# Kernel optimization log

Measured on AMD Instinct MI355X. Metric: run time of the kernel, lower is better.

The kernel has to match this reference:

```python
import jax, jax.numpy as jnp
import numpy as np

B, N, I, H, O, E, HD = 4, 2048, 32, 64, 32, 2, 2  # batch, nodes, in_dim, hidden, out, edgetypes, heads
D1 = H * HD * E  # layer-1 filter input dim (concat of all heads/edgetypes from layer 0)


def setup_inputs() -> dict:
    key = jax.random.key(0)
    ks = jax.random.split(key, 20)
    s = 0.1
    return {
        "nodes": jax.random.normal(ks[0], (B, N, I), jnp.float32),
        "edges": jax.random.normal(ks[1], (B, N, N, E), jnp.float32),
        "W_emb": jax.random.normal(ks[2], (I, H), jnp.float32) * s,
        "b_emb": jnp.zeros((H,), jnp.float32),
        "Wf0": jax.random.normal(ks[3], (E, HD, H, H), jnp.float32) * s,
        "w1_0": jax.random.normal(ks[4], (E, HD, H), jnp.float32) * s,
        "b1_0": jnp.zeros((E, HD), jnp.float32),
        "w2_0": jax.random.normal(ks[5], (E, HD, H), jnp.float32) * s,
        "b2_0": jnp.zeros((E, HD), jnp.float32),
        "bias0": jax.random.normal(ks[6], (HD, H), jnp.float32) * s,  # state_bias aliased across edgetypes (list-mult bug)
        "Wf1": jax.random.normal(ks[7], (E, HD, D1, H), jnp.float32) * s,
        "w1_1": jax.random.normal(ks[8], (E, HD, H), jnp.float32) * s,
        "b1_1": jnp.zeros((E, HD), jnp.float32),
        "w2_1": jax.random.normal(ks[9], (E, HD, H), jnp.float32) * s,
        "b2_1": jnp.zeros((E, HD), jnp.float32),
        "bias1": jax.random.normal(ks[10], (HD, H), jnp.float32) * s,
        "W_out": jax.random.normal(ks[11], (H, O), jnp.float32) * s,
        "b_out": jnp.zeros((O,), jnp.float32),
    }


def _gat_layer(state, Wf, w1, b1, w2, b2, bias, edges_t, last):
    # state: (B,N,Din); Wf: (E,HD,Din,H); edges_t: (E,B,N,N)
    Wh = jnp.einsum('bnd,ehdk->ehbnk', state, Wf)                     # (E,HD,B,N,H)
    a1 = jnp.einsum('ehbnk,ehk->ehbn', Wh, w1) + b1[:, :, None, None]
    a2 = jnp.einsum('ehbnk,ehk->ehbn', Wh, w2) + b2[:, :, None, None]
    logits = jax.nn.leaky_relu(a1[..., :, None] + a2[..., None, :], 0.2) + edges_t[:, None]
    att = jax.nn.softmax(logits, axis=-2)                             # torch softmax dim=1 (over rows)
    msg = jnp.einsum('ehbik,ehbkd->ehbid', att, Wh) + bias[None, :, None, None, :]
    if last:
        return jnp.mean(jax.nn.elu(msg), axis=(0, 1))                 # (B,N,H)
    # concat in (edgetype-major, head-minor) order, matching the python loops
    return jnp.transpose(msg, (2, 3, 0, 1, 4)).reshape(msg.shape[2], msg.shape[3], -1)


def reference(nodes, edges, W_emb, b_emb, Wf0, w1_0, b1_0, w2_0, b2_0, bias0,
              Wf1, w1_1, b1_1, w2_1, b2_1, bias1, W_out, b_out):
    edges_t = jnp.transpose(edges, (3, 0, 1, 2))                      # (E,B,N,N)
    state = nodes @ W_emb + b_emb                                     # embedding
    state = _gat_layer(state, Wf0, w1_0, b1_0, w2_0, b2_0, bias0, edges_t, last=False)
    state = _gat_layer(state, Wf1, w1_1, b1_1, w2_1, b2_1, bias1, edges_t, last=True)
    out = state @ W_out + b_out                                       # (B,N,O)
    return jnp.mean(out, axis=1)                                      # graph-level output (B,O)
```

## Files before the change

kernel.cpp:

```cpp
#include <hip/hip_runtime.h>
#include <hip/hip_bf16.h>


constexpr int B_  = 4;
constexpr int N_  = 2048;
constexpr int I_  = 32;
constexpr int H_  = 64;
constexpr int O_  = 32;
constexpr int EH_ = 4;
constexpr int D1_ = 256;
constexpr int BN_ = B_ * N_;
constexpr int NC_ = 16;
constexpr int CH_ = N_ / NC_;
constexpr int TI_ = 16;
constexpr int TK_ = 32;
constexpr int NKT_ = N_ / TK_;

typedef __bf16 bf16x8 __attribute__((ext_vector_type(8)));
typedef float floatx4 __attribute__((ext_vector_type(4)));

__device__ __forceinline__ unsigned short f2b(float f) {
    unsigned int u = __float_as_uint(f);
    return (unsigned short)((u + 0x7fffu + ((u >> 16) & 1u)) >> 16);
}
__device__ __forceinline__ float lrelu(float x) { return fmaxf(x, 0.2f * x); }

__global__ __launch_bounds__(256) void embed_kernel(
        const float* __restrict__ nodes, const float* __restrict__ W_emb,
        const float* __restrict__ b_emb, unsigned short* __restrict__ state0B) {
    int t = threadIdx.x;
    int r = t >> 6, h = t & 63;
    int bn = blockIdx.x * 4 + r;
    __shared__ float sn[4][I_];
    if (t < 4 * I_) {
        int rr = t / I_, ii = t % I_;
        sn[rr][ii] = nodes[(size_t)(blockIdx.x * 4 + rr) * I_ + ii];
    }
    __syncthreads();
    float acc = b_emb[h];
    #pragma unroll
    for (int i = 0; i < I_; ++i) acc += sn[r][i] * W_emb[i * H_ + h];
    state0B[(size_t)bn * H_ + h] = f2b(acc);
}

template <int DIN>
__global__ __launch_bounds__(256) void wf_pack_kernel(
        const float* __restrict__ Wf, unsigned short* __restrict__ WfB) {
    int o = blockIdx.x * 256 + threadIdx.x;
    int k = o & (DIN - 1);
    int n = (o / DIN) & 63;
    int c = o / (DIN * 64);
    WfB[o] = f2b(Wf[((size_t)c * DIN + k) * 64 + n]);
}

template <int DIN>
__global__ __launch_bounds__(256) void wh_a_mfma_kernel(
        const unsigned short* __restrict__ stateB, const unsigned short* __restrict__ WfB,
        const float* __restrict__ w1, const float* __restrict__ b1,
        const float* __restrict__ w2, const float* __restrict__ b2,
        unsigned short* __restrict__ WhB, float* __restrict__ a1,
        float* __restrict__ a2) {
    int t = threadIdx.x;
    int lane = t & 63, wv = t >> 6;
    int col = lane & 15, qd = lane >> 4;
    int bn0 = blockIdx.x * TI_;
    int b = bn0 >> 11;

    floatx4 acc[4] = {{0,0,0,0},{0,0,0,0},{0,0,0,0},{0,0,0,0}};
    const unsigned short* __restrict__ ap = stateB + (size_t)(bn0 + col) * DIN + qd * 8;
    const unsigned short* __restrict__ bp = WfB + ((size_t)(wv * 64 + col) * DIN + qd * 8);
    #pragma unroll
    for (int k0 = 0; k0 < DIN; k0 += 32) {
        bf16x8 af = *(const bf16x8*)(ap + k0);
        #pragma unroll
        for (int nt = 0; nt < 4; ++nt) {
            bf16x8 bf = *(const bf16x8*)(bp + (size_t)nt * 16 * DIN + k0);
            acc[nt] = __builtin_amdgcn_mfma_f32_16x16x32_bf16(af, bf, acc[nt], 0, 0, 0);
        }
    }
    int nb = ((bn0 & 2047) >> 3) + (qd >> 1);
    #pragma unroll
    for (int nt = 0; nt < 4; ++nt) {
        unsigned int lo = (unsigned int)f2b(acc[nt][0]) | ((unsigned int)f2b(acc[nt][1]) << 16);
        unsigned int hi = (unsigned int)f2b(acc[nt][2]) | ((unsigned int)f2b(acc[nt][3]) << 16);
        uint2 v = make_uint2(lo, hi);
        *(uint2*)(WhB + ((((size_t)(wv * B_ + b) * 256 + nb) * 64 + nt * 16 + col) * 8
                         + (qd & 1) * 4)) = v;
    }
    float p1[4] = {}, p2[4] = {};
    #pragma unroll
    for (int nt = 0; nt < 4; ++nt) {
        float w1n = w1[wv * H_ + nt * 16 + col];
        float w2n = w2[wv * H_ + nt * 16 + col];
        #pragma unroll
        for (int r = 0; r < 4; ++r) {
            p1[r] += acc[nt][r] * w1n;
            p2[r] += acc[nt][r] * w2n;
        }
    }
    #pragma unroll
    for (int m = 1; m < 16; m <<= 1)
        #pragma unroll
        for (int r = 0; r < 4; ++r) {
            p1[r] += __shfl_xor(p1[r], m, 64);
            p2[r] += __shfl_xor(p2[r], m, 64);
        }
    if (col == 0) {
        float b1c = b1[wv], b2c = b2[wv];
        #pragma unroll
        for (int r = 0; r < 4; ++r) {
            a1[(size_t)wv * BN_ + bn0 + qd * 4 + r] = p1[r] + b1c;
            a2[(size_t)wv * BN_ + bn0 + qd * 4 + r] = p2[r] + b2c;
        }
    }
}

__global__ __launch_bounds__(256) void stats_kernel(
        const float* __restrict__ edges, const float* __restrict__ a1,
        const float* __restrict__ a2, float* __restrict__ ps) {
    int blk = blockIdx.x;
    int jt = blk & 7;
    int ic = (blk >> 3) & (NC_ - 1);
    int b  = blk >> 7;
    int t = threadIdx.x;
    int j = jt * 256 + t;
    __shared__ float sa1[EH_][CH_];
    for (int q = t; q < EH_ * CH_; q += 256) {
        int cc = q / CH_, ii = q % CH_;
        sa1[cc][ii] = a1[(size_t)cc * BN_ + b * N_ + ic * CH_ + ii];
    }
    __syncthreads();
    float a2v[EH_], s[EH_] = {};
    #pragma unroll
    for (int cc = 0; cc < EH_; ++cc)
        a2v[cc] = a2[(size_t)cc * BN_ + b * N_ + j];
    const float2* __restrict__ ep = (const float2*)edges + ((size_t)(b * N_ + ic * CH_)) * N_ + j;
    for (int i0 = 0; i0 < CH_; i0 += 8) {
        float2 u[8];
        #pragma unroll
        for (int q = 0; q < 8; ++q) u[q] = ep[(size_t)(i0 + q) * N_];
        #pragma unroll
        for (int q = 0; q < 8; ++q) {
            #pragma unroll
            for (int cc = 0; cc < EH_; ++cc) {
                float x = sa1[cc][i0 + q] + a2v[cc];
                s[cc] += __expf(lrelu(x) + ((cc < 2) ? u[q].x : u[q].y));
            }
        }
    }
    #pragma unroll
    for (int cc = 0; cc < EH_; ++cc)
        ps[((size_t)ic * EH_ + cc) * BN_ + b * N_ + j] = s[cc];
}

__global__ __launch_bounds__(256) void combine_kernel(
        const float* __restrict__ ps, const float* __restrict__ a2,
        float2* __restrict__ za) {
    int q = blockIdx.x * 256 + threadIdx.x;
    float S = 0.f;
    #pragma unroll
    for (int ic = 0; ic < NC_; ++ic) S += ps[(size_t)ic * EH_ * BN_ + q];
    za[q] = make_float2(__logf(S), a2[q]);
}

template <int LAST>
__global__ __launch_bounds__(256, 4) void mac_kernel(
        const float* __restrict__ edges, const float* __restrict__ a1,
        const float2* __restrict__ za, const unsigned short* __restrict__ WhB,
        const float* __restrict__ bias, void* __restrict__ outv) {
    int t = threadIdx.x;
    int blk = blockIdx.x;
    int b = blk >> 7;
    int i0 = (blk & 127) * TI_;
    int lane = t & 63, wv = t >> 6;
    int ai = t >> 4;
    int ak = (t & 15) * 2;
    int qd = lane >> 4;
    int col = lane & 15;

    __shared__ unsigned short satt[2][EH_][TI_][40];
    __shared__ float2 szq[2][EH_][TK_];
    __shared__ float sred[EH_][TI_][H_];

    float a1v[EH_];
    #pragma unroll
    for (int cc = 0; cc < EH_; ++cc)
        a1v[cc] = a1[(size_t)cc * BN_ + b * N_ + i0 + ai];

    const float4* __restrict__ ep =
        (const float4*)edges + (size_t)(b * N_ + i0 + ai) * (N_ >> 1);
    float4 ev[4];
    #pragma unroll
    for (int q = 0; q < 4; ++q) ev[q] = ep[q * (TK_ >> 1) + (ak >> 1)];
    if (t < 128) {
        int cc = t >> 5, kk = t & 31;
        szq[0][cc][kk] = za[(size_t)cc * BN_ + b * N_ + kk];
    }
    const unsigned short* __restrict__ whb0 =
        WhB + (size_t)(wv * B_ + b) * (256 * 512);
    bf16x8 bcur[4], bnxt[4];
    #pragma unroll
    for (int nt = 0; nt < 4; ++nt)
        bcur[nt] = *(const bf16x8*)(whb0 + ((size_t)qd * 64 + nt * 16 + col) * 8);

    floatx4 acc[4] = {{0,0,0,0},{0,0,0,0},{0,0,0,0},{0,0,0,0}};
    __syncthreads();

    for (int kt = 0; kt < NKT_; ++kt) {
        int cur = kt & 1, nxt = cur ^ 1;
        int k0n = ((kt + 1) & (NKT_ - 1)) * TK_;
        if (t < 128) {
            int cc = t >> 5, kk = t & 31;
            szq[nxt][cc][kk] = za[(size_t)cc * BN_ + b * N_ + k0n + kk];
        }
        float4 e0 = ev[kt & 3];
        #pragma unroll
        for (int cc = 0; cc < EH_; ++cc) {
            float2 z0 = szq[cur][cc][ak];
            float2 z1 = szq[cur][cc][ak + 1];
            float ea = (cc < 2) ? e0.x : e0.y;
            float eb = (cc < 2) ? e0.z : e0.w;
            float at0 = __expf(lrelu(a1v[cc] + z0.y) + ea - z0.x);
            float at1 = __expf(lrelu(a1v[cc] + z1.y) + eb - z1.x);
            unsigned int p = (unsigned int)f2b(at0) | ((unsigned int)f2b(at1) << 16);
            *(unsigned int*)&satt[cur][cc][ai][ak] = p;
        }
        ev[kt & 3] = ep[((kt + 4) & (NKT_ - 1)) * (TK_ >> 1) + (ak >> 1)];
        __syncthreads();
        int kb = ((kt + 1) & (NKT_ - 1)) * (TK_ >> 3);
        #pragma unroll
        for (int nt = 0; nt < 4; ++nt)
            bnxt[nt] = *(const bf16x8*)(whb0 + ((size_t)(kb + qd) * 64 + nt * 16 + col) * 8);
        bf16x8 af = *(const bf16x8*)&satt[cur][wv][col][qd * 8];
        #pragma unroll
        for (int nt = 0; nt < 4; ++nt)
            acc[nt] = __builtin_amdgcn_mfma_f32_16x16x32_bf16(af, bcur[nt], acc[nt], 0, 0, 0);
        #pragma unroll
        for (int nt = 0; nt < 4; ++nt) bcur[nt] = bnxt[nt];
    }

    if (LAST) {
        float* out = (float*)outv;
        #pragma unroll
        for (int nt = 0; nt < 4; ++nt) {
            float bv = bias[(wv & 1) * H_ + nt * 16 + col];
            #pragma unroll
            for (int r = 0; r < 4; ++r) {
                float x = acc[nt][r] + bv;
                sred[wv][qd * 4 + r][nt * 16 + col] = x > 0.f ? x : (__expf(x) - 1.f);
            }
        }
        __syncthreads();
        #pragma unroll
        for (int q = 0; q < 4; ++q) {
            int p = t + q * 256;
            int r = p >> 6, d = p & 63;
            float s = sred[0][r][d] + sred[1][r][d] + sred[2][r][d] + sred[3][r][d];
            out[((size_t)(b * N_ + i0 + r)) * H_ + d] = s * 0.25f;
        }
    } else {
        unsigned short* out = (unsigned short*)outv;
        #pragma unroll
        for (int nt = 0; nt < 4; ++nt) {
            float bv = bias[(wv & 1) * H_ + nt * 16 + col];
            #pragma unroll
            for (int r = 0; r < 4; ++r)
                out[((size_t)(b * N_ + i0 + qd * 4 + r)) * D1_ + wv * H_ + nt * 16 + col] =
                    f2b(acc[nt][r] + bv);
        }
    }
}

__global__ __launch_bounds__(256) void out_kernel(
        const float* __restrict__ state2, const float* __restrict__ W_out,
        const float* __restrict__ b_out, float* __restrict__ out) {
    int b = blockIdx.x, t = threadIdx.x;
    int d = t & 63, nc = t >> 6;
    float psum = 0.f;
    const float* sp = state2 + ((size_t)b * N_ + nc * (N_ / 4)) * H_ + d;
    for (int n = 0; n < N_ / 4; ++n) psum += sp[(size_t)n * H_];
    __shared__ float red[4][H_];
    red[nc][d] = psum;
    __syncthreads();
    if (t < H_) red[0][d] = red[0][d] + red[1][d] + red[2][d] + red[3][d];
    __syncthreads();
    if (t < O_) {
        float acc = b_out[t];
        #pragma unroll 8
        for (int dd = 0; dd < H_; ++dd)
            acc += (red[0][dd] * (1.f / N_)) * W_out[dd * O_ + t];
        out[b * O_ + t] = acc;
    }
}

extern "C" void kernel_launch(void* const* d_in, const int* in_sizes, int n_in,
                              void* d_out, int out_size, void* d_ws, size_t ws_size,
                              hipStream_t stream) {
    const float* nodes = (const float*)d_in[0];
    const float* edges = (const float*)d_in[1];
    const float* W_emb = (const float*)d_in[2];
    const float* b_emb = (const float*)d_in[3];
    const float* Wf0   = (const float*)d_in[4];
    const float* w1_0  = (const float*)d_in[5];
    const float* b1_0  = (const float*)d_in[6];
    const float* w2_0  = (const float*)d_in[7];
    const float* b2_0  = (const float*)d_in[8];
    const float* bias0 = (const float*)d_in[9];
    const float* Wf1   = (const float*)d_in[10];
    const float* w1_1  = (const float*)d_in[11];
    const float* b1_1  = (const float*)d_in[12];
    const float* w2_1  = (const float*)d_in[13];
    const float* b2_1  = (const float*)d_in[14];
    const float* bias1 = (const float*)d_in[15];
    const float* W_out = (const float*)d_in[16];
    const float* b_out = (const float*)d_in[17];

    float* ws = (float*)d_ws;
    unsigned short* state0B = (unsigned short*)ws;
    unsigned short* state1B = (unsigned short*)(ws + 262144);
    float* state2 = ws + 262144 + 1048576;
    unsigned short* WhB  = (unsigned short*)(state2 + 524288);
    unsigned short* WfB0 = (unsigned short*)(state2 + 524288 + 1048576);
    unsigned short* WfB1 = WfB0 + 16384;
    float* a1   = state2 + 524288 + 1048576 + 8192 + 32768;
    float* a2   = a1 + 32768;
    float* psum = a2 + 32768;
    float2* za  = (float2*)(psum + 524288);

    wf_pack_kernel<H_><<<EH_ * 64 * H_ / 256, 256, 0, stream>>>(Wf0, WfB0);
    wf_pack_kernel<D1_><<<EH_ * 64 * D1_ / 256, 256, 0, stream>>>(Wf1, WfB1);
    embed_kernel<<<BN_ / 4, 256, 0, stream>>>(nodes, W_emb, b_emb, state0B);

    wh_a_mfma_kernel<H_><<<BN_ / TI_, 256, 0, stream>>>(state0B, WfB0, w1_0, b1_0,
                                                        w2_0, b2_0, WhB, a1, a2);
    stats_kernel<<<B_ * NC_ * (N_ / 256), 256, 0, stream>>>(edges, a1, a2, psum);
    combine_kernel<<<EH_ * BN_ / 256, 256, 0, stream>>>(psum, a2, za);
    mac_kernel<0><<<B_ * (N_ / TI_), 256, 0, stream>>>(edges, a1, za, WhB, bias0, state1B);
    wh_a_mfma_kernel<D1_><<<BN_ / TI_, 256, 0, stream>>>(state1B, WfB1, w1_1, b1_1,
                                                         w2_1, b2_1, WhB, a1, a2);
    stats_kernel<<<B_ * NC_ * (N_ / 256), 256, 0, stream>>>(edges, a1, a2, psum);
    combine_kernel<<<EH_ * BN_ / 256, 256, 0, stream>>>(psum, a2, za);
    mac_kernel<1><<<B_ * (N_ / TI_), 256, 0, stream>>>(edges, a1, za, WhB, bias1, state2);

    out_kernel<<<B_, 256, 0, stream>>>(state2, W_out, b_out, (float*)d_out);
}
```

Baseline: 462.0 us.

## Fold softmax normalizer into Wh and compute attention directly in MFMA registers

The column-softmax denominator exp(-Z_k) is folded into the bf16 Wh rows by a new scaling kernel, so the MAC loop no longer subtracts Z per element. Each wave now builds its own attention fragment in registers from edges and a2, which removes the shared-memory staging of attention tiles and the per-iteration __syncthreads. It also adds a four-deep register prefetch pipeline (occupancy hint lowered to 2) and doubles the stats chunk count for more parallelism. The trade-off is an extra rounding of Wh to bf16 after scaling, higher register pressure, and each wave rereading edges for its own head.

```diff
diff --git a/kernel.cpp b/kernel.cpp
--- a/kernel.cpp
+++ b/kernel.cpp
@@ -10,7 +10,7 @@
 constexpr int EH_ = 4;
 constexpr int D1_ = 256;
 constexpr int BN_ = B_ * N_;
-constexpr int NC_ = 16;
+constexpr int NC_ = 32;
 constexpr int CH_ = N_ / NC_;
 constexpr int TI_ = 16;
 constexpr int TK_ = 32;
@@ -121,12 +121,12 @@
     int blk = blockIdx.x;
     int jt = blk & 7;
     int ic = (blk >> 3) & (NC_ - 1);
-    int b  = blk >> 7;
+    int b  = blk >> 8;
     int t = threadIdx.x;
     int j = jt * 256 + t;
     __shared__ float sa1[EH_][CH_];
-    for (int q = t; q < EH_ * CH_; q += 256) {
-        int cc = q / CH_, ii = q % CH_;
+    if (t < EH_ * CH_) {
+        int cc = t / CH_, ii = t % CH_;
         sa1[cc][ii] = a1[(size_t)cc * BN_ + b * N_ + ic * CH_ + ii];
     }
     __syncthreads();
@@ -154,89 +154,109 @@
 }
 
 __global__ __launch_bounds__(256) void combine_kernel(
-        const float* __restrict__ ps, const float* __restrict__ a2,
-        float2* __restrict__ za) {
+        const float* __restrict__ ps, float* __restrict__ Z) {
     int q = blockIdx.x * 256 + threadIdx.x;
     float S = 0.f;
     #pragma unroll
     for (int ic = 0; ic < NC_; ++ic) S += ps[(size_t)ic * EH_ * BN_ + q];
-    za[q] = make_float2(__logf(S), a2[q]);
+    Z[q] = __logf(S);
+}
+
+__global__ __launch_bounds__(256) void scale_whb_kernel(
+        unsigned short* __restrict__ WhB, const float* __restrict__ Z) {
+    int gw = blockIdx.x * 4 + (threadIdx.x >> 6);
+    int lane = threadIdx.x & 63;
+    int kb = gw & 255;
+    int cb = gw >> 8;
+    int c = cb >> 2, b = cb & 3;
+    const float* zp = Z + (size_t)c * BN_ + b * N_ + kb * 8;
+    float sc[8];
+    #pragma unroll
+    for (int j = 0; j < 8; ++j) sc[j] = __expf(-zp[j]);
+    size_t base = ((size_t)cb * 256 + kb) * 512 + lane * 8;
+    union { unsigned short s[8]; uint4 v; } pk;
+    pk.v = *(const uint4*)(WhB + base);
+    #pragma unroll
+    for (int j = 0; j < 8; ++j) {
+        float f = __uint_as_float((unsigned int)pk.s[j] << 16) * sc[j];
+        pk.s[j] = f2b(f);
+    }
+    *(uint4*)(WhB + base) = pk.v;
+}
+
+__device__ __forceinline__ void mac_load(
+        int kt, const float4* __restrict__ ep, const float4* __restrict__ ap2,
+        const unsigned short* __restrict__ whb, int qd, int col,
+        float4 ev[4], float4 av[2], bf16x8 bb[4]) {
+    int kw = kt & (NKT_ - 1);
+    const float4* e = ep + kw * 16;
+    ev[0] = e[0]; ev[1] = e[1]; ev[2] = e[2]; ev[3] = e[3];
+    const float4* a = ap2 + kw * 8;
+    av[0] = a[0]; av[1] = a[1];
+    const unsigned short* w = whb + ((size_t)(kw * 4 + qd) * 64 + col) * 8;
+    bb[0] = *(const bf16x8*)(w);
+    bb[1] = *(const bf16x8*)(w + 128);
+    bb[2] = *(const bf16x8*)(w + 256);
+    bb[3] = *(const bf16x8*)(w + 384);
+}
+
+__device__ __forceinline__ void mac_compute(
+        float a1v, int esel, const float4 ev[4], const float4 av[2],
+        const bf16x8 bb[4], floatx4 acc[4]) {
+    const float* f = (const float*)ev;
+    const float* g = (const float*)av;
+    float p[8];
+    #pragma unroll
+    for (int j = 0; j < 8; ++j) {
+        float x = a1v + g[j];
+        p[j] = __expf(lrelu(x) + f[2 * j + esel]);
+    }
+    union { unsigned int u[4]; bf16x8 v; } af;
+    #pragma unroll
+    for (int j = 0; j < 4; ++j)
+        af.u[j] = (unsigned int)f2b(p[2 * j]) | ((unsigned int)f2b(p[2 * j + 1]) << 16);
+    #pragma unroll
+    for (int nt = 0; nt < 4; ++nt)
+        acc[nt] = __builtin_amdgcn_mfma_f32_16x16x32_bf16(af.v, bb[nt], acc[nt], 0, 0, 0);
 }
 
 template <int LAST>
-__global__ __launch_bounds__(256, 4) void mac_kernel(
+__global__ __launch_bounds__(256, 2) void mac_kernel(
         const float* __restrict__ edges, const float* __restrict__ a1,
-        const float2* __restrict__ za, const unsigned short* __restrict__ WhB,
+        const float* __restrict__ a2, const unsigned short* __restrict__ WhB,
         const float* __restrict__ bias, void* __restrict__ outv) {
     int t = threadIdx.x;
     int blk = blockIdx.x;
     int b = blk >> 7;
     int i0 = (blk & 127) * TI_;
     int lane = t & 63, wv = t >> 6;
-    int ai = t >> 4;
-    int ak = (t & 15) * 2;
     int qd = lane >> 4;
     int col = lane & 15;
-
-    __shared__ unsigned short satt[2][EH_][TI_][40];
-    __shared__ float2 szq[2][EH_][TK_];
+    int esel = (wv < 2) ? 0 : 1;
+
     __shared__ float sred[EH_][TI_][H_];
 
-    float a1v[EH_];
-    #pragma unroll
-    for (int cc = 0; cc < EH_; ++cc)
-        a1v[cc] = a1[(size_t)cc * BN_ + b * N_ + i0 + ai];
-
+    float a1v = a1[(size_t)wv * BN_ + b * N_ + i0 + col];
     const float4* __restrict__ ep =
-        (const float4*)edges + (size_t)(b * N_ + i0 + ai) * (N_ >> 1);
-    float4 ev[4];
-    #pragma unroll
-    for (int q = 0; q < 4; ++q) ev[q] = ep[q * (TK_ >> 1) + (ak >> 1)];
-    if (t < 128) {
-        int cc = t >> 5, kk = t & 31;
-        szq[0][cc][kk] = za[(size_t)cc * BN_ + b * N_ + kk];
-    }
-    const unsigned short* __restrict__ whb0 =
+        (const float4*)edges + (((size_t)(b * N_ + i0 + col) * N_) >> 1) + qd * 4;
+    const float4* __restrict__ ap2 =
+        (const float4*)(a2 + (size_t)wv * BN_ + b * N_) + qd * 2;
+    const unsigned short* __restrict__ whb =
         WhB + (size_t)(wv * B_ + b) * (256 * 512);
-    bf16x8 bcur[4], bnxt[4];
-    #pragma unroll
-    for (int nt = 0; nt < 4; ++nt)
-        bcur[nt] = *(const bf16x8*)(whb0 + ((size_t)qd * 64 + nt * 16 + col) * 8);
-
+
+    float4 ev[4][4]; float4 av[4][2]; bf16x8 bb[4][4];
     floatx4 acc[4] = {{0,0,0,0},{0,0,0,0},{0,0,0,0},{0,0,0,0}};
-    __syncthreads();
-
-    for (int kt = 0; kt < NKT_; ++kt) {
-        int cur = kt & 1, nxt = cur ^ 1;
-        int k0n = ((kt + 1) & (NKT_ - 1)) * TK_;
-        if (t < 128) {
-            int cc = t >> 5, kk = t & 31;
-            szq[nxt][cc][kk] = za[(size_t)cc * BN_ + b * N_ + k0n + kk];
-        }
-        float4 e0 = ev[kt & 3];
-        #pragma unroll
-        for (int cc = 0; cc < EH_; ++cc) {
-            float2 z0 = szq[cur][cc][ak];
-            float2 z1 = szq[cur][cc][ak + 1];
-            float ea = (cc < 2) ? e0.x : e0.y;
-            float eb = (cc < 2) ? e0.z : e0.w;
-            float at0 = __expf(lrelu(a1v[cc] + z0.y) + ea - z0.x);
-            float at1 = __expf(lrelu(a1v[cc] + z1.y) + eb - z1.x);
-            unsigned int p = (unsigned int)f2b(at0) | ((unsigned int)f2b(at1) << 16);
-            *(unsigned int*)&satt[cur][cc][ai][ak] = p;
-        }
-        ev[kt & 3] = ep[((kt + 4) & (NKT_ - 1)) * (TK_ >> 1) + (ak >> 1)];
-        __syncthreads();
-        int kb = ((kt + 1) & (NKT_ - 1)) * (TK_ >> 3);
-        #pragma unroll
-        for (int nt = 0; nt < 4; ++nt)
-            bnxt[nt] = *(const bf16x8*)(whb0 + ((size_t)(kb + qd) * 64 + nt * 16 + col) * 8);
-        bf16x8 af = *(const bf16x8*)&satt[cur][wv][col][qd * 8];
-        #pragma unroll
-        for (int nt = 0; nt < 4; ++nt)
-            acc[nt] = __builtin_amdgcn_mfma_f32_16x16x32_bf16(af, bcur[nt], acc[nt], 0, 0, 0);
-        #pragma unroll
-        for (int nt = 0; nt < 4; ++nt) bcur[nt] = bnxt[nt];
+
+    #pragma unroll
+    for (int ph = 0; ph < 4; ++ph)
+        mac_load(ph, ep, ap2, whb, qd, col, ev[ph], av[ph], bb[ph]);
+
+    for (int kt = 0; kt < NKT_; kt += 4) {
+        #pragma unroll
+        for (int ph = 0; ph < 4; ++ph) {
+            mac_compute(a1v, esel, ev[ph], av[ph], bb[ph], acc);
+            mac_load(kt + 4 + ph, ep, ap2, whb, qd, col, ev[ph], av[ph], bb[ph]);
+        }
     }
 
     if (LAST) {
@@ -325,7 +345,7 @@
     float* a1   = state2 + 524288 + 1048576 + 8192 + 32768;
     float* a2   = a1 + 32768;
     float* psum = a2 + 32768;
-    float2* za  = (float2*)(psum + 524288);
+    float* Zc   = psum + 1048576;
 
     wf_pack_kernel<H_><<<EH_ * 64 * H_ / 256, 256, 0, stream>>>(Wf0, WfB0);
     wf_pack_kernel<D1_><<<EH_ * 64 * D1_ / 256, 256, 0, stream>>>(Wf1, WfB1);
@@ -334,13 +354,15 @@
     wh_a_mfma_kernel<H_><<<BN_ / TI_, 256, 0, stream>>>(state0B, WfB0, w1_0, b1_0,
                                                         w2_0, b2_0, WhB, a1, a2);
     stats_kernel<<<B_ * NC_ * (N_ / 256), 256, 0, stream>>>(edges, a1, a2, psum);
-    combine_kernel<<<EH_ * BN_ / 256, 256, 0, stream>>>(psum, a2, za);
-    mac_kernel<0><<<B_ * (N_ / TI_), 256, 0, stream>>>(edges, a1, za, WhB, bias0, state1B);
+    combine_kernel<<<EH_ * BN_ / 256, 256, 0, stream>>>(psum, Zc);
+    scale_whb_kernel<<<EH_ * B_ * 256 / 4, 256, 0, stream>>>(WhB, Zc);
+    mac_kernel<0><<<B_ * (N_ / TI_), 256, 0, stream>>>(edges, a1, a2, WhB, bias0, state1B);
     wh_a_mfma_kernel<D1_><<<BN_ / TI_, 256, 0, stream>>>(state1B, WfB1, w1_1, b1_1,
                                                          w2_1, b2_1, WhB, a1, a2);
     stats_kernel<<<B_ * NC_ * (N_ / 256), 256, 0, stream>>>(edges, a1, a2, psum);
-    combine_kernel<<<EH_ * BN_ / 256, 256, 0, stream>>>(psum, a2, za);
-    mac_kernel<1><<<B_ * (N_ / TI_), 256, 0, stream>>>(edges, a1, za, WhB, bias1, state2);
+    combine_kernel<<<EH_ * BN_ / 256, 256, 0, stream>>>(psum, Zc);
+    scale_whb_kernel<<<EH_ * B_ * 256 / 4, 256, 0, stream>>>(WhB, Zc);
+    mac_kernel<1><<<B_ * (N_ / TI_), 256, 0, stream>>>(edges, a1, a2, WhB, bias1, state2);
 
     out_kernel<<<B_, 256, 0, stream>>>(state2, W_out, b_out, (float*)d_out);
 }
```

After: 770.9 us. 66.9% more time.
